# Kernel tuning notes

Hardware: AMD Instinct MI355X
Metric: run time of the kernel (lower is better)

Reference implementation:

```python
import jax, jax.numpy as jnp
import numpy as np

N_NODES = 80000
N_EDGES = 1280000
N_FEAT = 4
HIDDEN = 64
N_CLASSES = 2
N_GRAPHS = 64
BN_EPS = 1e-5


def setup_inputs() -> dict:
    key = jax.random.key(0)
    ks = jax.random.split(key, 16)
    x = jax.random.normal(ks[0], (N_NODES, N_FEAT), dtype=jnp.float32)
    edge_index = jax.random.randint(ks[1], (2, N_EDGES), 0, N_NODES, dtype=jnp.int64)
    batch = jnp.sort(jax.random.randint(ks[2], (N_NODES,), 0, N_GRAPHS, dtype=jnp.int64))

    def lin_w(k, fan_in, fan_out):
        bound = 1.0 / np.sqrt(fan_in)
        return jax.random.uniform(k, (fan_in, fan_out), jnp.float32, -bound, bound)

    inp = {
        "x": x, "edge_index": edge_index, "batch": batch,
        # BatchNorm1d (eval mode: running stats)
        "bn_gamma": jnp.ones((N_FEAT,), jnp.float32),
        "bn_beta": jnp.zeros((N_FEAT,), jnp.float32),
        "bn_mean": jnp.zeros((N_FEAT,), jnp.float32),
        "bn_var": jnp.ones((N_FEAT,), jnp.float32),
        # GraphConv layers: out = agg @ W_rel + b_rel + x @ W_root
        "W1_rel": lin_w(ks[3], N_FEAT, HIDDEN), "b1_rel": jnp.zeros((HIDDEN,), jnp.float32),
        "W1_root": lin_w(ks[4], N_FEAT, HIDDEN),
        "W2_rel": lin_w(ks[5], HIDDEN, HIDDEN), "b2_rel": jnp.zeros((HIDDEN,), jnp.float32),
        "W2_root": lin_w(ks[6], HIDDEN, HIDDEN),
        "W3_rel": lin_w(ks[7], HIDDEN, HIDDEN), "b3_rel": jnp.zeros((HIDDEN,), jnp.float32),
        "W3_root": lin_w(ks[8], HIDDEN, HIDDEN),
        "lin_W": lin_w(ks[9], HIDDEN, N_CLASSES),
        "lin_b": jnp.zeros((N_CLASSES,), jnp.float32),
    }
    return inp


def _graph_conv(x, src, dst, W_rel, b_rel, W_root):
    # PyG GraphConv: x_i' = W_root x_i + W_rel * sum_{j in N(i)} x_j + b_rel
    agg = jax.ops.segment_sum(x[src], dst, num_segments=N_NODES)  # [N, C_in]
    return agg @ W_rel + b_rel + x @ W_root


def reference(x, edge_index, batch,
              bn_gamma, bn_beta, bn_mean, bn_var,
              W1_rel, b1_rel, W1_root,
              W2_rel, b2_rel, W2_root,
              W3_rel, b3_rel, W3_root,
              lin_W, lin_b):
    src, dst = edge_index[0], edge_index[1]
    # BatchNorm1d, eval mode (running stats); dropout is a no-op in eval.
    h = (x - bn_mean) * (bn_gamma * jax.lax.rsqrt(bn_var + BN_EPS)) + bn_beta
    h = jax.nn.relu(_graph_conv(h, src, dst, W1_rel, b1_rel, W1_root))
    h = jax.nn.relu(_graph_conv(h, src, dst, W2_rel, b2_rel, W2_root))
    h = _graph_conv(h, src, dst, W3_rel, b3_rel, W3_root)
    # global mean pool over graphs
    sums = jax.ops.segment_sum(h, batch, num_segments=N_GRAPHS)        # [G, H]
    cnts = jax.ops.segment_sum(jnp.ones((h.shape[0],), h.dtype), batch,
                               num_segments=N_GRAPHS)                  # [G]
    pooled = sums / jnp.maximum(cnts, 1.0)[:, None]
    return pooled @ lin_W + lin_b  # [G, num_classes]
```

## Files before the change

### kernel.cpp

```cpp
#include <hip/hip_runtime.h>
#include <hip/hip_bf16.h>

#define N_NODES 80000
#define N_EDGES 1280000
#define N_FEAT 4
#define HIDDEN 64
#define N_GRAPHS 64
#define BN_EPS 1e-5f

#define NBUCK 313
#define BCAP 8000
#define EPT 16

typedef unsigned short ushort_t;
typedef __attribute__((ext_vector_type(8))) short bf16x8;
typedef __attribute__((ext_vector_type(4))) float f32x4;

__device__ __forceinline__ float bf2f(ushort_t v) {
    return __uint_as_float(((unsigned)v) << 16);
}
__device__ __forceinline__ ushort_t f2bf(float f) {
    unsigned u = __float_as_uint(f);
    u += 0x7FFFu + ((u >> 16) & 1u);
    return (ushort_t)(u >> 16);
}

__global__ void wprep_kernel(const float* __restrict__ W2_rel,
                             const float* __restrict__ W2_root,
                             const float* __restrict__ W3_rel,
                             const float* __restrict__ W3_root,
                             ushort_t* __restrict__ WcatT2,
                             ushort_t* __restrict__ WcatT3,
                             int* __restrict__ bcursor,
                             float* __restrict__ pool,
                             float* __restrict__ cnt,
                             int* __restrict__ done) {
    int i = blockIdx.x * blockDim.x + threadIdx.x;
    int which = i >= 64 * 128;
    int j = i & (64 * 128 - 1);
    int n = j >> 7, k = j & 127;
    const float* Wr = which ? W3_rel : W2_rel;
    const float* Wo = which ? W3_root : W2_root;
    ushort_t* Wc = which ? WcatT3 : WcatT2;
    float w = (k < 64) ? Wr[k * 64 + n] : Wo[(k - 64) * 64 + n];
    Wc[j] = f2bf(w);
    if (i < 4096) pool[i] = 0.f;
    else if (i < 4160) cnt[i - 4096] = 0.f;
    else if (i < 4160 + NBUCK) bcursor[i - 4160] = 0;
    else if (i == 4160 + NBUCK) *done = 0;
}

__global__ __launch_bounds__(256) void bucket_kernel(
        const int* __restrict__ src, const int* __restrict__ dst,
        unsigned* __restrict__ pairs, int* __restrict__ bcursor) {
    __shared__ int hist[NBUCK];
    __shared__ int base[NBUCK];
    for (int i = threadIdx.x; i < NBUCK; i += 256) hist[i] = 0;
    __syncthreads();
    const int e0 = blockIdx.x * (256 * EPT) + threadIdx.x;
    int d[EPT], r[EPT];
#pragma unroll
    for (int k = 0; k < EPT; ++k) {
        int e = e0 + k * 256;
        if (e < N_EDGES) {
            d[k] = dst[e];
            r[k] = atomicAdd(&hist[d[k] >> 8], 1);
        }
    }
    __syncthreads();
    for (int i = threadIdx.x; i < NBUCK; i += 256) {
        int c = hist[i];
        base[i] = c ? atomicAdd(&bcursor[i], c) : 0;
    }
    __syncthreads();
#pragma unroll
    for (int k = 0; k < EPT; ++k) {
        int e = e0 + k * 256;
        if (e < N_EDGES) {
            int b = d[k] >> 8;
            int pos = base[b] + r[k];
            if (pos < BCAP)
                pairs[(size_t)b * BCAP + pos] =
                    (unsigned)src[e] | (((unsigned)d[k] & 255u) << 17);
        }
    }
}

__global__ __launch_bounds__(256) void csr_build_kernel(
        const unsigned* __restrict__ pairs, const int* __restrict__ bcursor,
        int* __restrict__ rowstart, int* __restrict__ csr) {
    __shared__ int degl[256];
    __shared__ int pref[256];
    __shared__ int curs[256];
    const int b = blockIdx.x;
    const int t = threadIdx.x;
    int partial = 0;
    for (int i = t; i < b; i += 256) partial += min(bcursor[i], BCAP);
    pref[t] = partial;
    __syncthreads();
    for (int off = 128; off > 0; off >>= 1) {
        if (t < off) pref[t] += pref[t + off];
        __syncthreads();
    }
    const int base = pref[0];
    const int cntb = min(bcursor[b], BCAP);
    __syncthreads();
    degl[t] = 0;
    __syncthreads();
    const unsigned* pb = pairs + (size_t)b * BCAP;
    for (int i = t; i < cntb; i += 256) {
        atomicAdd(&degl[pb[i] >> 17], 1);
    }
    __syncthreads();
    int v = degl[t];
    pref[t] = v;
    __syncthreads();
    for (int off = 1; off < 256; off <<= 1) {
        int u = (t >= off) ? pref[t - off] : 0;
        __syncthreads();
        pref[t] += u;
        __syncthreads();
    }
    int excl = pref[t] - v;
    int node = b * 256 + t;
    if (node < N_NODES) rowstart[node] = base + excl;
    if (b == NBUCK - 1 && t == 255) rowstart[N_NODES] = base + cntb;
    curs[t] = excl;
    __syncthreads();
    for (int i = t; i < cntb; i += 256) {
        unsigned p = pb[i];
        int pos = atomicAdd(&curs[p >> 17], 1);
        csr[base + pos] = (int)(p & 0x1FFFFu);
    }
}

__global__ __launch_bounds__(1024) void layer1_kernel(
        const float* __restrict__ x, ushort_t* __restrict__ h1,
        const int* __restrict__ rowstart, const int* __restrict__ csr,
        const float* __restrict__ Wrel, const float* __restrict__ Wroot,
        const float* __restrict__ b,
        const float* __restrict__ gamma, const float* __restrict__ beta,
        const float* __restrict__ mean, const float* __restrict__ var) {
    const int lane = threadIdx.x & 63;
    const int wid = threadIdx.x >> 6;
    float scale[4], shift[4];
#pragma unroll
    for (int k = 0; k < 4; ++k) {
        float sc = gamma[k] * rsqrtf(var[k] + BN_EPS);
        scale[k] = sc;
        shift[k] = beta[k] - mean[k] * sc;
    }
    float wrel2[4], wroot2[4];
    float crel = 0.f, croot = 0.f;
#pragma unroll
    for (int k = 0; k < 4; ++k) {
        float wr = Wrel[k * 64 + lane], wo = Wroot[k * 64 + lane];
        wrel2[k] = scale[k] * wr;  crel += shift[k] * wr;
        wroot2[k] = scale[k] * wo; croot += shift[k] * wo;
    }
    const float bj = b[lane] + croot;
    const int sub = lane >> 2;
    const int f = lane & 3;
    const int nW = gridDim.x * 16;
    for (int n0 = blockIdx.x * 16 + wid; n0 < N_NODES; n0 += nW) {
        const int node = __builtin_amdgcn_readfirstlane(n0);
        const int e0 = rowstart[node], e1 = rowstart[node + 1];
        const float deg = (float)(e1 - e0);
        float part = 0.f;
        for (int e = e0 + sub; e < e1; e += 16) {
            int s = csr[e];
            part += x[s * 4 + f];
        }
        part += __shfl_xor(part, 4);
        part += __shfl_xor(part, 8);
        part += __shfl_xor(part, 16);
        part += __shfl_xor(part, 32);
        float a0 = __shfl(part, 0), a1 = __shfl(part, 1);
        float a2 = __shfl(part, 2), a3 = __shfl(part, 3);
        float x0 = x[node * 4 + 0], x1 = x[node * 4 + 1];
        float x2 = x[node * 4 + 2], x3 = x[node * 4 + 3];
        float out = bj + deg * crel
                  + a0 * wrel2[0] + a1 * wrel2[1] + a2 * wrel2[2] + a3 * wrel2[3]
                  + x0 * wroot2[0] + x1 * wroot2[1] + x2 * wroot2[2] + x3 * wroot2[3];
        h1[(size_t)node * 64 + lane] = f2bf(fmaxf(out, 0.f));
    }
}

__global__ __launch_bounds__(256) void gather_kernel(
        const ushort_t* __restrict__ hin, ushort_t* __restrict__ Gagg,
        const int* __restrict__ rowstart, const int* __restrict__ csr) {
    const int lane = threadIdx.x & 63;
    const int node = __builtin_amdgcn_readfirstlane(blockIdx.x * 4 + (threadIdx.x >> 6));
    const int e0 = rowstart[node], e1 = rowstart[node + 1];
    float a0 = 0.f, a1 = 0.f, a2 = 0.f, a3 = 0.f;
    float a4 = 0.f, a5 = 0.f, a6 = 0.f, a7 = 0.f;
    int e = e0;
    for (; e + 16 <= e1; e += 16) {
        int idx = csr[e + (lane & 15)];
        int s0 = __builtin_amdgcn_readlane(idx, 0);
        int s1 = __builtin_amdgcn_readlane(idx, 1);
        int s2 = __builtin_amdgcn_readlane(idx, 2);
        int s3 = __builtin_amdgcn_readlane(idx, 3);
        int s4 = __builtin_amdgcn_readlane(idx, 4);
        int s5 = __builtin_amdgcn_readlane(idx, 5);
        int s6 = __builtin_amdgcn_readlane(idx, 6);
        int s7 = __builtin_amdgcn_readlane(idx, 7);
        int s8 = __builtin_amdgcn_readlane(idx, 8);
        int s9 = __builtin_amdgcn_readlane(idx, 9);
        int s10 = __builtin_amdgcn_readlane(idx, 10);
        int s11 = __builtin_amdgcn_readlane(idx, 11);
        int s12 = __builtin_amdgcn_readlane(idx, 12);
        int s13 = __builtin_amdgcn_readlane(idx, 13);
        int s14 = __builtin_amdgcn_readlane(idx, 14);
        int s15 = __builtin_amdgcn_readlane(idx, 15);
        ushort_t v0 = hin[(size_t)s0 * 64 + lane];
        ushort_t v1 = hin[(size_t)s1 * 64 + lane];
        ushort_t v2 = hin[(size_t)s2 * 64 + lane];
        ushort_t v3 = hin[(size_t)s3 * 64 + lane];
        ushort_t v4 = hin[(size_t)s4 * 64 + lane];
        ushort_t v5 = hin[(size_t)s5 * 64 + lane];
        ushort_t v6 = hin[(size_t)s6 * 64 + lane];
        ushort_t v7 = hin[(size_t)s7 * 64 + lane];
        ushort_t v8 = hin[(size_t)s8 * 64 + lane];
        ushort_t v9 = hin[(size_t)s9 * 64 + lane];
        ushort_t v10 = hin[(size_t)s10 * 64 + lane];
        ushort_t v11 = hin[(size_t)s11 * 64 + lane];
        ushort_t v12 = hin[(size_t)s12 * 64 + lane];
        ushort_t v13 = hin[(size_t)s13 * 64 + lane];
        ushort_t v14 = hin[(size_t)s14 * 64 + lane];
        ushort_t v15 = hin[(size_t)s15 * 64 + lane];
        a0 += bf2f(v0) + bf2f(v8);
        a1 += bf2f(v1) + bf2f(v9);
        a2 += bf2f(v2) + bf2f(v10);
        a3 += bf2f(v3) + bf2f(v11);
        a4 += bf2f(v4) + bf2f(v12);
        a5 += bf2f(v5) + bf2f(v13);
        a6 += bf2f(v6) + bf2f(v14);
        a7 += bf2f(v7) + bf2f(v15);
    }
    if (e + 8 <= e1) {
        int idx = csr[e + (lane & 7)];
        int s0 = __builtin_amdgcn_readlane(idx, 0);
        int s1 = __builtin_amdgcn_readlane(idx, 1);
        int s2 = __builtin_amdgcn_readlane(idx, 2);
        int s3 = __builtin_amdgcn_readlane(idx, 3);
        int s4 = __builtin_amdgcn_readlane(idx, 4);
        int s5 = __builtin_amdgcn_readlane(idx, 5);
        int s6 = __builtin_amdgcn_readlane(idx, 6);
        int s7 = __builtin_amdgcn_readlane(idx, 7);
        ushort_t v0 = hin[(size_t)s0 * 64 + lane];
        ushort_t v1 = hin[(size_t)s1 * 64 + lane];
        ushort_t v2 = hin[(size_t)s2 * 64 + lane];
        ushort_t v3 = hin[(size_t)s3 * 64 + lane];
        ushort_t v4 = hin[(size_t)s4 * 64 + lane];
        ushort_t v5 = hin[(size_t)s5 * 64 + lane];
        ushort_t v6 = hin[(size_t)s6 * 64 + lane];
        ushort_t v7 = hin[(size_t)s7 * 64 + lane];
        a0 += bf2f(v0); a1 += bf2f(v1); a2 += bf2f(v2); a3 += bf2f(v3);
        a4 += bf2f(v4); a5 += bf2f(v5); a6 += bf2f(v6); a7 += bf2f(v7);
        e += 8;
    }
    if (e + 4 <= e1) {
        int idx = csr[e + (lane & 3)];
        int s0 = __builtin_amdgcn_readlane(idx, 0);
        int s1 = __builtin_amdgcn_readlane(idx, 1);
        int s2 = __builtin_amdgcn_readlane(idx, 2);
        int s3 = __builtin_amdgcn_readlane(idx, 3);
        ushort_t v0 = hin[(size_t)s0 * 64 + lane];
        ushort_t v1 = hin[(size_t)s1 * 64 + lane];
        ushort_t v2 = hin[(size_t)s2 * 64 + lane];
        ushort_t v3 = hin[(size_t)s3 * 64 + lane];
        a0 += bf2f(v0); a1 += bf2f(v1); a2 += bf2f(v2); a3 += bf2f(v3);
        e += 4;
    }
    for (; e < e1; ++e) {
        int s = __builtin_amdgcn_readfirstlane(csr[e]);
        a0 += bf2f(hin[(size_t)s * 64 + lane]);
    }
    float agg = ((a0 + a1) + (a2 + a3)) + ((a4 + a5) + (a6 + a7));
    Gagg[(size_t)node * 64 + lane] = f2bf(agg);
}

__global__ __launch_bounds__(256) void gemm_kernel(
        const ushort_t* __restrict__ Gagg, const ushort_t* __restrict__ hin,
        ushort_t* __restrict__ hout,
        const ushort_t* __restrict__ WcatT, const float* __restrict__ b,
        int relu) {
    const int lane = threadIdx.x & 63;
    const int col = lane & 15;
    const int grp = lane >> 4;

    bf16x8 bf[4][4];
#pragma unroll
    for (int kt = 0; kt < 4; ++kt)
#pragma unroll
        for (int nt = 0; nt < 4; ++nt)
            bf[kt][nt] = *(const bf16x8*)&WcatT[(nt * 16 + col) * 128 + kt * 32 + grp * 8];

    float bj[4];
#pragma unroll
    for (int nt = 0; nt < 4; ++nt) bj[nt] = b[nt * 16 + col];

    const int tile = blockIdx.x * 4 + (threadIdx.x >> 6);
    if (tile >= N_NODES / 16) return;
    const int node0 = tile * 16;

    const ushort_t* ga = Gagg + (size_t)(node0 + col) * 64 + grp * 8;
    const ushort_t* ha = hin + (size_t)(node0 + col) * 64 + grp * 8;
    f32x4 acc0 = {0.f, 0.f, 0.f, 0.f};
    f32x4 acc1 = {0.f, 0.f, 0.f, 0.f};
    f32x4 acc2 = {0.f, 0.f, 0.f, 0.f};
    f32x4 acc3 = {0.f, 0.f, 0.f, 0.f};
#pragma unroll
    for (int kt = 0; kt < 4; ++kt) {
        bf16x8 a = (kt < 2) ? *(const bf16x8*)(ga + kt * 32)
                            : *(const bf16x8*)(ha + (kt - 2) * 32);
        acc0 = __builtin_amdgcn_mfma_f32_16x16x32_bf16(a, bf[kt][0], acc0, 0, 0, 0);
        acc1 = __builtin_amdgcn_mfma_f32_16x16x32_bf16(a, bf[kt][1], acc1, 0, 0, 0);
        acc2 = __builtin_amdgcn_mfma_f32_16x16x32_bf16(a, bf[kt][2], acc2, 0, 0, 0);
        acc3 = __builtin_amdgcn_mfma_f32_16x16x32_bf16(a, bf[kt][3], acc3, 0, 0, 0);
    }

#pragma unroll
    for (int nt = 0; nt < 4; ++nt) {
        f32x4 acc = (nt == 0) ? acc0 : (nt == 1) ? acc1 : (nt == 2) ? acc2 : acc3;
        const int c = nt * 16 + col;
#pragma unroll
        for (int r = 0; r < 4; ++r) {
            int row = grp * 4 + r;
            float v = acc[r] + bj[nt];
            if (relu) v = fmaxf(v, 0.f);
            hout[(size_t)(node0 + row) * 64 + c] = f2bf(v);
        }
    }
}

__global__ __launch_bounds__(256) void pool_head_kernel(
        const ushort_t* __restrict__ h3, const int* __restrict__ batch,
        float* __restrict__ pool, float* __restrict__ cnt, int* __restrict__ done,
        const float* __restrict__ linW, const float* __restrict__ linb,
        float* __restrict__ out) {
    const int lane = threadIdx.x & 63;
    const int gw = (blockIdx.x * blockDim.x + threadIdx.x) >> 6;
    const int nW = (gridDim.x * blockDim.x) >> 6;
    const int chunk = (N_NODES + nW - 1) / nW;
    int n0 = gw * chunk;
    int n1 = n0 + chunk; if (n1 > N_NODES) n1 = N_NODES;
    if (n0 < N_NODES) {
        float acc = 0.f;
        int cur = batch[n0];
        int cl = 0;
#define POOL_FLUSH() do { atomicAdd(&pool[cur * 64 + lane], acc); \
        if (lane == 0) atomicAdd(&cnt[cur], (float)cl); acc = 0.f; cl = 0; } while (0)
        int n = n0;
        for (; n + 8 <= n1; n += 8) {
            float v0 = bf2f(h3[(size_t)(n + 0) * 64 + lane]);
            float v1 = bf2f(h3[(size_t)(n + 1) * 64 + lane]);
            float v2 = bf2f(h3[(size_t)(n + 2) * 64 + lane]);
            float v3 = bf2f(h3[(size_t)(n + 3) * 64 + lane]);
            float v4 = bf2f(h3[(size_t)(n + 4) * 64 + lane]);
            float v5 = bf2f(h3[(size_t)(n + 5) * 64 + lane]);
            float v6 = bf2f(h3[(size_t)(n + 6) * 64 + lane]);
            float v7 = bf2f(h3[(size_t)(n + 7) * 64 + lane]);
            int g0 = batch[n + 0], g1 = batch[n + 1], g2 = batch[n + 2], g3 = batch[n + 3];
            int g4 = batch[n + 4], g5 = batch[n + 5], g6 = batch[n + 6], g7 = batch[n + 7];
            if (g0 != cur) { POOL_FLUSH(); cur = g0; } acc += v0; cl++;
            if (g1 != cur) { POOL_FLUSH(); cur = g1; } acc += v1; cl++;
            if (g2 != cur) { POOL_FLUSH(); cur = g2; } acc += v2; cl++;
            if (g3 != cur) { POOL_FLUSH(); cur = g3; } acc += v3; cl++;
            if (g4 != cur) { POOL_FLUSH(); cur = g4; } acc += v4; cl++;
            if (g5 != cur) { POOL_FLUSH(); cur = g5; } acc += v5; cl++;
            if (g6 != cur) { POOL_FLUSH(); cur = g6; } acc += v6; cl++;
            if (g7 != cur) { POOL_FLUSH(); cur = g7; } acc += v7; cl++;
        }
        for (; n < n1; ++n) {
            int g = batch[n];
            if (g != cur) { POOL_FLUSH(); cur = g; }
            acc += bf2f(h3[(size_t)n * 64 + lane]);
            cl++;
        }
        atomicAdd(&pool[cur * 64 + lane], acc);
        if (lane == 0) atomicAdd(&cnt[cur], (float)cl);
#undef POOL_FLUSH
    }
    __threadfence();
    __syncthreads();
    __shared__ int lastFlag;
    if (threadIdx.x == 0) {
        int t = atomicAdd(done, 1);
        lastFlag = (t == (int)gridDim.x - 1);
    }
    __syncthreads();
    if (lastFlag) {
        __threadfence();
        int g = threadIdx.x >> 1;
        int c = threadIdx.x & 1;
        if (threadIdx.x < 128) {
            float inv = 1.0f / fmaxf(cnt[g], 1.0f);
            float acc = linb[c];
            for (int j = 0; j < 64; ++j) acc += pool[g * 64 + j] * inv * linW[j * 2 + c];
            out[g * 2 + c] = acc;
        }
    }
}

extern "C" void kernel_launch(void* const* d_in, const int* in_sizes, int n_in,
                              void* d_out, int out_size, void* d_ws, size_t ws_size,
                              hipStream_t stream) {
    const float* x = (const float*)d_in[0];
    const int* edge_index = (const int*)d_in[1];
    const int* batch = (const int*)d_in[2];
    const float* bn_gamma = (const float*)d_in[3];
    const float* bn_beta = (const float*)d_in[4];
    const float* bn_mean = (const float*)d_in[5];
    const float* bn_var = (const float*)d_in[6];
    const float* W1_rel = (const float*)d_in[7];
    const float* b1_rel = (const float*)d_in[8];
    const float* W1_root = (const float*)d_in[9];
    const float* W2_rel = (const float*)d_in[10];
    const float* b2_rel = (const float*)d_in[11];
    const float* W2_root = (const float*)d_in[12];
    const float* W3_rel = (const float*)d_in[13];
    const float* b3_rel = (const float*)d_in[14];
    const float* W3_root = (const float*)d_in[15];
    const float* lin_W = (const float*)d_in[16];
    const float* lin_b = (const float*)d_in[17];
    float* out = (float*)d_out;

    const int* e_src = edge_index;
    const int* e_dst = edge_index + N_EDGES;

    ushort_t* h1 = (ushort_t*)d_ws;
    ushort_t* h2 = h1 + 5120000;
    float* pool = (float*)(h2 + 5120000);
    float* cnt = pool + 4096;
    int* bcursor = (int*)(cnt + 64);
    int* done = bcursor + 316;
    int* rowstart = bcursor + 320 + 320;
    int* csr = rowstart + 80016;
    ushort_t* WcatT2 = (ushort_t*)(csr + 1280000);
    ushort_t* WcatT3 = WcatT2 + 8192;
    ushort_t* Gagg = (ushort_t*)(WcatT3 + 8192 + 16);
    unsigned* pairs = (unsigned*)h1;
    ushort_t* h3 = h1;

    wprep_kernel<<<64, 256, 0, stream>>>(W2_rel, W2_root, W3_rel, W3_root,
                                         WcatT2, WcatT3, bcursor, pool, cnt, done);

    bucket_kernel<<<(N_EDGES + 256 * EPT - 1) / (256 * EPT), 256, 0, stream>>>(
        e_src, e_dst, pairs, bcursor);
    csr_build_kernel<<<NBUCK, 256, 0, stream>>>(pairs, bcursor, rowstart, csr);

    layer1_kernel<<<512, 1024, 0, stream>>>(x, h1, rowstart, csr, W1_rel, W1_root,
                                            b1_rel, bn_gamma, bn_beta, bn_mean, bn_var);

    gather_kernel<<<N_NODES / 4, 256, 0, stream>>>(h1, Gagg, rowstart, csr);
    gemm_kernel<<<N_NODES / 64, 256, 0, stream>>>(Gagg, h1, h2, WcatT2, b2_rel, 1);

    gather_kernel<<<N_NODES / 4, 256, 0, stream>>>(h2, Gagg, rowstart, csr);
    gemm_kernel<<<N_NODES / 64, 256, 0, stream>>>(Gagg, h2, h3, WcatT3, b3_rel, 0);

    pool_head_kernel<<<256, 256, 0, stream>>>(h3, batch, pool, cnt, done,
                                              lin_W, lin_b, out);
}
```

Before: 182.9 us.

## Gather two edges per wavefront with 32-bit loads; split pool and head kernels

The gather kernel now splits each wavefront into two halves. Each half handles a different neighbour edge and loads packed bf16 pairs as 32-bit words, so one load instruction covers two edges' full rows. A cross-half shuffle combines the partial sums and a packed store writes the result. This is meant to halve the number of load instructions and raise memory-level parallelism in the dominant gather phase. Separately, the last-block-done atomic pattern in the pool kernel is replaced by a separate tiny head kernel, which removes a fence and atomic counter but adds one launch.

```diff
diff --git a/kernel.cpp b/kernel.cpp
--- a/kernel.cpp
+++ b/kernel.cpp
@@ -33,8 +33,7 @@
                              ushort_t* __restrict__ WcatT3,
                              int* __restrict__ bcursor,
                              float* __restrict__ pool,
-                             float* __restrict__ cnt,
-                             int* __restrict__ done) {
+                             float* __restrict__ cnt) {
     int i = blockIdx.x * blockDim.x + threadIdx.x;
     int which = i >= 64 * 128;
     int j = i & (64 * 128 - 1);
@@ -47,7 +46,6 @@
     if (i < 4096) pool[i] = 0.f;
     else if (i < 4160) cnt[i - 4096] = 0.f;
     else if (i < 4160 + NBUCK) bcursor[i - 4160] = 0;
-    else if (i == 4160 + NBUCK) *done = 0;
 }
 
 __global__ __launch_bounds__(256) void bucket_kernel(
@@ -190,95 +188,68 @@
         const ushort_t* __restrict__ hin, ushort_t* __restrict__ Gagg,
         const int* __restrict__ rowstart, const int* __restrict__ csr) {
     const int lane = threadIdx.x & 63;
+    const int l = lane & 31;
+    const int half = lane >> 5;
     const int node = __builtin_amdgcn_readfirstlane(blockIdx.x * 4 + (threadIdx.x >> 6));
     const int e0 = rowstart[node], e1 = rowstart[node + 1];
-    float a0 = 0.f, a1 = 0.f, a2 = 0.f, a3 = 0.f;
-    float a4 = 0.f, a5 = 0.f, a6 = 0.f, a7 = 0.f;
+    float ax[8], ay[8];
+#pragma unroll
+    for (int k = 0; k < 8; ++k) { ax[k] = 0.f; ay[k] = 0.f; }
     int e = e0;
     for (; e + 16 <= e1; e += 16) {
         int idx = csr[e + (lane & 15)];
-        int s0 = __builtin_amdgcn_readlane(idx, 0);
-        int s1 = __builtin_amdgcn_readlane(idx, 1);
-        int s2 = __builtin_amdgcn_readlane(idx, 2);
-        int s3 = __builtin_amdgcn_readlane(idx, 3);
-        int s4 = __builtin_amdgcn_readlane(idx, 4);
-        int s5 = __builtin_amdgcn_readlane(idx, 5);
-        int s6 = __builtin_amdgcn_readlane(idx, 6);
-        int s7 = __builtin_amdgcn_readlane(idx, 7);
-        int s8 = __builtin_amdgcn_readlane(idx, 8);
-        int s9 = __builtin_amdgcn_readlane(idx, 9);
-        int s10 = __builtin_amdgcn_readlane(idx, 10);
-        int s11 = __builtin_amdgcn_readlane(idx, 11);
-        int s12 = __builtin_amdgcn_readlane(idx, 12);
-        int s13 = __builtin_amdgcn_readlane(idx, 13);
-        int s14 = __builtin_amdgcn_readlane(idx, 14);
-        int s15 = __builtin_amdgcn_readlane(idx, 15);
-        ushort_t v0 = hin[(size_t)s0 * 64 + lane];
-        ushort_t v1 = hin[(size_t)s1 * 64 + lane];
-        ushort_t v2 = hin[(size_t)s2 * 64 + lane];
-        ushort_t v3 = hin[(size_t)s3 * 64 + lane];
-        ushort_t v4 = hin[(size_t)s4 * 64 + lane];
-        ushort_t v5 = hin[(size_t)s5 * 64 + lane];
-        ushort_t v6 = hin[(size_t)s6 * 64 + lane];
-        ushort_t v7 = hin[(size_t)s7 * 64 + lane];
-        ushort_t v8 = hin[(size_t)s8 * 64 + lane];
-        ushort_t v9 = hin[(size_t)s9 * 64 + lane];
-        ushort_t v10 = hin[(size_t)s10 * 64 + lane];
-        ushort_t v11 = hin[(size_t)s11 * 64 + lane];
-        ushort_t v12 = hin[(size_t)s12 * 64 + lane];
-        ushort_t v13 = hin[(size_t)s13 * 64 + lane];
-        ushort_t v14 = hin[(size_t)s14 * 64 + lane];
-        ushort_t v15 = hin[(size_t)s15 * 64 + lane];
-        a0 += bf2f(v0) + bf2f(v8);
-        a1 += bf2f(v1) + bf2f(v9);
-        a2 += bf2f(v2) + bf2f(v10);
-        a3 += bf2f(v3) + bf2f(v11);
-        a4 += bf2f(v4) + bf2f(v12);
-        a5 += bf2f(v5) + bf2f(v13);
-        a6 += bf2f(v6) + bf2f(v14);
-        a7 += bf2f(v7) + bf2f(v15);
+#pragma unroll
+        for (int k = 0; k < 8; ++k) {
+            int s = __shfl(idx, 2 * k + half);
+            unsigned rp = *(const unsigned*)&hin[(size_t)s * 64 + 2 * l];
+            ax[k] += __uint_as_float(rp << 16);
+            ay[k] += __uint_as_float(rp & 0xFFFF0000u);
+        }
     }
     if (e + 8 <= e1) {
         int idx = csr[e + (lane & 7)];
-        int s0 = __builtin_amdgcn_readlane(idx, 0);
-        int s1 = __builtin_amdgcn_readlane(idx, 1);
-        int s2 = __builtin_amdgcn_readlane(idx, 2);
-        int s3 = __builtin_amdgcn_readlane(idx, 3);
-        int s4 = __builtin_amdgcn_readlane(idx, 4);
-        int s5 = __builtin_amdgcn_readlane(idx, 5);
-        int s6 = __builtin_amdgcn_readlane(idx, 6);
-        int s7 = __builtin_amdgcn_readlane(idx, 7);
-        ushort_t v0 = hin[(size_t)s0 * 64 + lane];
-        ushort_t v1 = hin[(size_t)s1 * 64 + lane];
-        ushort_t v2 = hin[(size_t)s2 * 64 + lane];
-        ushort_t v3 = hin[(size_t)s3 * 64 + lane];
-        ushort_t v4 = hin[(size_t)s4 * 64 + lane];
-        ushort_t v5 = hin[(size_t)s5 * 64 + lane];
-        ushort_t v6 = hin[(size_t)s6 * 64 + lane];
-        ushort_t v7 = hin[(size_t)s7 * 64 + lane];
-        a0 += bf2f(v0); a1 += bf2f(v1); a2 += bf2f(v2); a3 += bf2f(v3);
-        a4 += bf2f(v4); a5 += bf2f(v5); a6 += bf2f(v6); a7 += bf2f(v7);
+#pragma unroll
+        for (int k = 0; k < 4; ++k) {
+            int s = __shfl(idx, 2 * k + half);
+            unsigned rp = *(const unsigned*)&hin[(size_t)s * 64 + 2 * l];
+            ax[k] += __uint_as_float(rp << 16);
+            ay[k] += __uint_as_float(rp & 0xFFFF0000u);
+        }
         e += 8;
     }
     if (e + 4 <= e1) {
         int idx = csr[e + (lane & 3)];
-        int s0 = __builtin_amdgcn_readlane(idx, 0);
-        int s1 = __builtin_amdgcn_readlane(idx, 1);
-        int s2 = __builtin_amdgcn_readlane(idx, 2);
-        int s3 = __builtin_amdgcn_readlane(idx, 3);
-        ushort_t v0 = hin[(size_t)s0 * 64 + lane];
-        ushort_t v1 = hin[(size_t)s1 * 64 + lane];
-        ushort_t v2 = hin[(size_t)s2 * 64 + lane];
-        ushort_t v3 = hin[(size_t)s3 * 64 + lane];
-        a0 += bf2f(v0); a1 += bf2f(v1); a2 += bf2f(v2); a3 += bf2f(v3);
+#pragma unroll
+        for (int k = 0; k < 2; ++k) {
+            int s = __shfl(idx, 2 * k + half);
+            unsigned rp = *(const unsigned*)&hin[(size_t)s * 64 + 2 * l];
+            ax[k] += __uint_as_float(rp << 16);
+            ay[k] += __uint_as_float(rp & 0xFFFF0000u);
+        }
         e += 4;
     }
-    for (; e < e1; ++e) {
+    if (e + 2 <= e1) {
+        int idx = csr[e + (lane & 1)];
+        int s = __shfl(idx, half);
+        unsigned rp = *(const unsigned*)&hin[(size_t)s * 64 + 2 * l];
+        ax[0] += __uint_as_float(rp << 16);
+        ay[0] += __uint_as_float(rp & 0xFFFF0000u);
+        e += 2;
+    }
+    if (e < e1 && half == 0) {
         int s = __builtin_amdgcn_readfirstlane(csr[e]);
-        a0 += bf2f(hin[(size_t)s * 64 + lane]);
-    }
-    float agg = ((a0 + a1) + (a2 + a3)) + ((a4 + a5) + (a6 + a7));
-    Gagg[(size_t)node * 64 + lane] = f2bf(agg);
+        unsigned rp = *(const unsigned*)&hin[(size_t)s * 64 + 2 * l];
+        ax[0] += __uint_as_float(rp << 16);
+        ay[0] += __uint_as_float(rp & 0xFFFF0000u);
+    }
+    float fx = ((ax[0] + ax[1]) + (ax[2] + ax[3])) + ((ax[4] + ax[5]) + (ax[6] + ax[7]));
+    float fy = ((ay[0] + ay[1]) + (ay[2] + ay[3])) + ((ay[4] + ay[5]) + (ay[6] + ay[7]));
+    fx += __shfl_xor(fx, 32);
+    fy += __shfl_xor(fy, 32);
+    if (lane < 32) {
+        unsigned ap = (unsigned)f2bf(fx) | ((unsigned)f2bf(fy) << 16);
+        ((unsigned*)(Gagg + (size_t)node * 64))[l] = ap;
+    }
 }
 
 __global__ __launch_bounds__(256) void gemm_kernel(
@@ -335,72 +306,62 @@
     }
 }
 
-__global__ __launch_bounds__(256) void pool_head_kernel(
-        const ushort_t* __restrict__ h3, const int* __restrict__ batch,
-        float* __restrict__ pool, float* __restrict__ cnt, int* __restrict__ done,
-        const float* __restrict__ linW, const float* __restrict__ linb,
-        float* __restrict__ out) {
+__global__ void pool_kernel(const ushort_t* __restrict__ h3, const int* __restrict__ batch,
+                            float* __restrict__ pool, float* __restrict__ cnt) {
     const int lane = threadIdx.x & 63;
     const int gw = (blockIdx.x * blockDim.x + threadIdx.x) >> 6;
     const int nW = (gridDim.x * blockDim.x) >> 6;
     const int chunk = (N_NODES + nW - 1) / nW;
     int n0 = gw * chunk;
     int n1 = n0 + chunk; if (n1 > N_NODES) n1 = N_NODES;
-    if (n0 < N_NODES) {
-        float acc = 0.f;
-        int cur = batch[n0];
-        int cl = 0;
+    if (n0 >= N_NODES) return;
+    float acc = 0.f;
+    int cur = batch[n0];
+    int cl = 0;
 #define POOL_FLUSH() do { atomicAdd(&pool[cur * 64 + lane], acc); \
         if (lane == 0) atomicAdd(&cnt[cur], (float)cl); acc = 0.f; cl = 0; } while (0)
-        int n = n0;
-        for (; n + 8 <= n1; n += 8) {
-            float v0 = bf2f(h3[(size_t)(n + 0) * 64 + lane]);
-            float v1 = bf2f(h3[(size_t)(n + 1) * 64 + lane]);
-            float v2 = bf2f(h3[(size_t)(n + 2) * 64 + lane]);
-            float v3 = bf2f(h3[(size_t)(n + 3) * 64 + lane]);
-            float v4 = bf2f(h3[(size_t)(n + 4) * 64 + lane]);
-            float v5 = bf2f(h3[(size_t)(n + 5) * 64 + lane]);
-            float v6 = bf2f(h3[(size_t)(n + 6) * 64 + lane]);
-            float v7 = bf2f(h3[(size_t)(n + 7) * 64 + lane]);
-            int g0 = batch[n + 0], g1 = batch[n + 1], g2 = batch[n + 2], g3 = batch[n + 3];
-            int g4 = batch[n + 4], g5 = batch[n + 5], g6 = batch[n + 6], g7 = batch[n + 7];
-            if (g0 != cur) { POOL_FLUSH(); cur = g0; } acc += v0; cl++;
-            if (g1 != cur) { POOL_FLUSH(); cur = g1; } acc += v1; cl++;
-            if (g2 != cur) { POOL_FLUSH(); cur = g2; } acc += v2; cl++;
-            if (g3 != cur) { POOL_FLUSH(); cur = g3; } acc += v3; cl++;
-            if (g4 != cur) { POOL_FLUSH(); cur = g4; } acc += v4; cl++;
-            if (g5 != cur) { POOL_FLUSH(); cur = g5; } acc += v5; cl++;
-            if (g6 != cur) { POOL_FLUSH(); cur = g6; } acc += v6; cl++;
-            if (g7 != cur) { POOL_FLUSH(); cur = g7; } acc += v7; cl++;
-        }
-        for (; n < n1; ++n) {
-            int g = batch[n];
-            if (g != cur) { POOL_FLUSH(); cur = g; }
-            acc += bf2f(h3[(size_t)n * 64 + lane]);
-            cl++;
-        }
-        atomicAdd(&pool[cur * 64 + lane], acc);
-        if (lane == 0) atomicAdd(&cnt[cur], (float)cl);
+    int n = n0;
+    for (; n + 8 <= n1; n += 8) {
+        float v0 = bf2f(h3[(size_t)(n + 0) * 64 + lane]);
+        float v1 = bf2f(h3[(size_t)(n + 1) * 64 + lane]);
+        float v2 = bf2f(h3[(size_t)(n + 2) * 64 + lane]);
+        float v3 = bf2f(h3[(size_t)(n + 3) * 64 + lane]);
+        float v4 = bf2f(h3[(size_t)(n + 4) * 64 + lane]);
+        float v5 = bf2f(h3[(size_t)(n + 5) * 64 + lane]);
+        float v6 = bf2f(h3[(size_t)(n + 6) * 64 + lane]);
+        float v7 = bf2f(h3[(size_t)(n + 7) * 64 + lane]);
+        int g0 = batch[n + 0], g1 = batch[n + 1], g2 = batch[n + 2], g3 = batch[n + 3];
+        int g4 = batch[n + 4], g5 = batch[n + 5], g6 = batch[n + 6], g7 = batch[n + 7];
+        if (g0 != cur) { POOL_FLUSH(); cur = g0; } acc += v0; cl++;
+        if (g1 != cur) { POOL_FLUSH(); cur = g1; } acc += v1; cl++;
+        if (g2 != cur) { POOL_FLUSH(); cur = g2; } acc += v2; cl++;
+        if (g3 != cur) { POOL_FLUSH(); cur = g3; } acc += v3; cl++;
+        if (g4 != cur) { POOL_FLUSH(); cur = g4; } acc += v4; cl++;
+        if (g5 != cur) { POOL_FLUSH(); cur = g5; } acc += v5; cl++;
+        if (g6 != cur) { POOL_FLUSH(); cur = g6; } acc += v6; cl++;
+        if (g7 != cur) { POOL_FLUSH(); cur = g7; } acc += v7; cl++;
+    }
+    for (; n < n1; ++n) {
+        int g = batch[n];
+        if (g != cur) { POOL_FLUSH(); cur = g; }
+        acc += bf2f(h3[(size_t)n * 64 + lane]);
+        cl++;
+    }
+    atomicAdd(&pool[cur * 64 + lane], acc);
+    if (lane == 0) atomicAdd(&cnt[cur], (float)cl);
 #undef POOL_FLUSH
-    }
-    __threadfence();
-    __syncthreads();
-    __shared__ int lastFlag;
-    if (threadIdx.x == 0) {
-        int t = atomicAdd(done, 1);
-        lastFlag = (t == (int)gridDim.x - 1);
-    }
-    __syncthreads();
-    if (lastFlag) {
-        __threadfence();
-        int g = threadIdx.x >> 1;
-        int c = threadIdx.x & 1;
-        if (threadIdx.x < 128) {
-            float inv = 1.0f / fmaxf(cnt[g], 1.0f);
-            float acc = linb[c];
-            for (int j = 0; j < 64; ++j) acc += pool[g * 64 + j] * inv * linW[j * 2 + c];
-            out[g * 2 + c] = acc;
-        }
+}
+
+__global__ void head_kernel(const float* __restrict__ pool, const float* __restrict__ cnt,
+                            const float* __restrict__ linW, const float* __restrict__ linb,
+                            float* __restrict__ out) {
+    int g = threadIdx.x >> 1;
+    int c = threadIdx.x & 1;
+    if (g < N_GRAPHS) {
+        float inv = 1.0f / fmaxf(cnt[g], 1.0f);
+        float acc = linb[c];
+        for (int j = 0; j < 64; ++j) acc += pool[g * 64 + j] * inv * linW[j * 2 + c];
+        out[g * 2 + c] = acc;
     }
 }
 
@@ -435,8 +396,7 @@
     float* pool = (float*)(h2 + 5120000);
     float* cnt = pool + 4096;
     int* bcursor = (int*)(cnt + 64);
-    int* done = bcursor + 316;
-    int* rowstart = bcursor + 320 + 320;
+    int* rowstart = bcursor + 640;
     int* csr = rowstart + 80016;
     ushort_t* WcatT2 = (ushort_t*)(csr + 1280000);
     ushort_t* WcatT3 = WcatT2 + 8192;
@@ -445,7 +405,7 @@
     ushort_t* h3 = h1;
 
     wprep_kernel<<<64, 256, 0, stream>>>(W2_rel, W2_root, W3_rel, W3_root,
-                                         WcatT2, WcatT3, bcursor, pool, cnt, done);
+                                         WcatT2, WcatT3, bcursor, pool, cnt);
 
     bucket_kernel<<<(N_EDGES + 256 * EPT - 1) / (256 * EPT), 256, 0, stream>>>(
         e_src, e_dst, pairs, bcursor);
@@ -460,6 +420,6 @@
     gather_kernel<<<N_NODES / 4, 256, 0, stream>>>(h2, Gagg, rowstart, csr);
     gemm_kernel<<<N_NODES / 64, 256, 0, stream>>>(Gagg, h2, h3, WcatT3, b3_rel, 0);
 
-    pool_head_kernel<<<256, 256, 0, stream>>>(h3, batch, pool, cnt, done,
-                                              lin_W, lin_b, out);
-}
+    pool_kernel<<<256, 256, 0, stream>>>(h3, batch, pool, cnt);
+    head_kernel<<<1, 128, 0, stream>>>(pool, cnt, lin_W, lin_b, out);
+}
```

New measurement: 171.5 us. -6.2%, faster.
